# Optimization experiments

Hardware: AMD Instinct MI355X
Metric: run time of the kernel (lower is better)

The kernel has to match this reference:

```python
import jax, jax.numpy as jnp
import numpy as np

TEMPERATURE = 8.0  # sqrt(head_dim=64)


def setup_inputs() -> dict:
    key = jax.random.key(0)
    kq, kk, kv, km = jax.random.split(key, 4)
    B, S, D = 16, 2048, 64
    q = jax.random.normal(kq, (B, S, D), dtype=jnp.float32)
    k = jax.random.normal(kk, (B, S, D), dtype=jnp.float32)
    v = jax.random.normal(kv, (B, S, D), dtype=jnp.float32)
    mask = jax.random.randint(km, (B, S, S), 0, 2).astype(jnp.bool_)
    return {"q": q, "k": k, "v": v, "mask": mask}


def reference(q, k, v, mask):
    # latent = q @ k^T / temperature  -> [B, Sq, Sk]
    latent = jnp.einsum('bqd,bkd->bqk', q, k) / TEMPERATURE
    # NOTE: the original fills masked positions with 1e-9 (NOT -inf); keep faithful.
    latent = jnp.where(mask, jnp.float32(1e-9), latent)
    attn = jax.nn.softmax(latent, axis=-1)
    return jnp.einsum('bqk,bkd->bqd', attn, v)
```

## Files before the change

### kernel.cpp

```cpp
#include <hip/hip_runtime.h>
#include <hip/hip_bf16.h>

#define BB 16
#define SS 2048
#define DD 64

typedef __attribute__((ext_vector_type(8)))  unsigned short ushort8;
typedef __attribute__((ext_vector_type(8)))  __bf16 bf16x8;
typedef __attribute__((ext_vector_type(16))) float f32x16;

static __device__ __forceinline__ unsigned short f2bf(float x) {
    return __builtin_bit_cast(unsigned short, __float2bfloat16(x));
}
static __device__ __forceinline__ unsigned pk2(float a, float b) {
    return (unsigned)f2bf(a) | ((unsigned)f2bf(b) << 16);
}
union F4 { float4 v; float a[4]; };

__global__ __launch_bounds__(256, 4)
void sdpa_mfma_kernel(const float* __restrict__ Q, const float* __restrict__ K,
                      const float* __restrict__ V, const unsigned int* __restrict__ M,
                      float* __restrict__ O) {
    __shared__ __align__(16) char smem[37120];
    char* Ks = smem;
    char* Vs = smem + 16384;
    char* Ms = smem + 32768;
    char* Qs = smem + 32768;
    float* red  = (float*)smem;
    float* denx = (float*)(smem + 32768);

    const int t    = threadIdx.x;
    const int lane = t & 63;
    const int l31  = lane & 31;
    const int half = lane >> 5;
    const int kh   = t >> 6;
    const int b    = blockIdx.y;
    const int q0   = blockIdx.x * 32;

    const float* Kg = K + (size_t)b * SS * DD;
    const float* Vg = V + (size_t)b * SS * DD;
    const unsigned int* Mg = M + (size_t)b * SS * SS + (size_t)q0 * SS;

    {
        const int sr = t >> 3, sc = t & 7;
        const float* src = Q + ((size_t)b * SS + q0 + sr) * DD + sc * 8;
        F4 f0, f1; f0.v = *(const float4*)src; f1.v = *(const float4*)(src + 4);
        ushort8 u;
        #pragma unroll
        for (int e = 0; e < 4; e++) {
            u[e]     = f2bf(f0.a[e] * 0.125f);
            u[e + 4] = f2bf(f1.a[e] * 0.125f);
        }
        *(ushort8*)(Qs + sr * 128 + ((sc ^ (sr & 7)) * 16)) = u;
    }
    __syncthreads();

    const int qrow = l31;
    bf16x8 bq[4];
    #pragma unroll
    for (int dc = 0; dc < 4; dc++)
        bq[dc] = __builtin_bit_cast(bf16x8, *(const ushort8*)(
            Qs + qrow * 128 + (((2 * dc + half) ^ (qrow & 7)) * 16)));
    __syncthreads();

    f32x16 On0, On1;
    #pragma unroll
    for (int i = 0; i < 16; i++) { On0[i] = 0.f; On1[i] = 0.f; }
    float den_acc = 0.f;

    const int krow = 32 * kh + l31;
    const int d0v  = (t & 15) * 4;
    const int kkb  = (t >> 4) * 4;

    for (int kt = 0; kt < SS / 128; ++kt) {
        #pragma unroll
        for (int j = 0; j < 4; j++) {
            const int idx = 2 * t + 512 * j;
            const int row = idx >> 4;
            const int g   = (idx & 15) >> 1;
            const float* src = Kg + (size_t)(kt * 128) * DD + (size_t)idx * 4;
            F4 fa, fb; fa.v = *(const float4*)src; fb.v = *(const float4*)(src + 4);
            ushort8 u;
            #pragma unroll
            for (int e = 0; e < 4; e++) { u[e] = f2bf(fa.a[e]); u[e + 4] = f2bf(fb.a[e]); }
            *(ushort8*)(Ks + row * 128 + ((g ^ (row & 7)) * 16)) = u;
        }
        #pragma unroll
        for (int it2 = 0; it2 < 2; it2++) {
            const int kk = kkb + 64 * it2;
            const float* src = Vg + (size_t)(kt * 128 + kk) * DD + d0v;
            F4 r0, r1, r2, r3;
            r0.v = *(const float4*)(src);
            r1.v = *(const float4*)(src + DD);
            r2.v = *(const float4*)(src + 2 * DD);
            r3.v = *(const float4*)(src + 3 * DD);
            #pragma unroll
            for (int e = 0; e < 4; e++) {
                const int d = d0v + e;
                const uint2 wv = make_uint2(pk2(r0.a[e], r1.a[e]), pk2(r2.a[e], r3.a[e]));
                *(uint2*)(Vs + d * 256 + (((kk >> 3) ^ (d & 15)) * 16) + (kk & 7) * 2) = wv;
            }
        }
        {
            const int sr = t >> 3, sc = t & 7;
            const unsigned int* Mw = Mg + (size_t)sr * SS + kt * 128 + sc * 16;
            unsigned wd[4];
            #pragma unroll
            for (int g = 0; g < 4; g++) {
                const uint4 u = *(const uint4*)(Mw + 4 * g);
                wd[g] = (u.x ? 1u : 0u) | (u.y ? 0x100u : 0u) |
                        (u.z ? 0x10000u : 0u) | (u.w ? 0x1000000u : 0u);
            }
            *(uint2*)(Ms + sr * 136 + sc * 16)     = make_uint2(wd[0], wd[1]);
            *(uint2*)(Ms + sr * 136 + sc * 16 + 8) = make_uint2(wd[2], wd[3]);
        }
        __syncthreads();

        f32x16 S;
        #pragma unroll
        for (int i = 0; i < 16; i++) S[i] = 0.f;
        #pragma unroll
        for (int dc = 0; dc < 4; dc++) {
            bf16x8 ak = __builtin_bit_cast(bf16x8, *(const ushort8*)(
                Ks + krow * 128 + (((2 * dc + half) ^ (krow & 7)) * 16)));
            S = __builtin_amdgcn_mfma_f32_32x32x16_bf16(ak, bq[dc], S, 0, 0, 0);
        }

        float p[16];
        #pragma unroll
        for (int g = 0; g < 4; g++) {
            const unsigned mw = *(const unsigned*)(Ms + qrow * 136 + 32 * kh + 8 * g + 4 * half);
            #pragma unroll
            for (int e = 0; e < 4; e++) {
                const float ev = __expf(S[4 * g + e]);
                const float pv = ((mw >> (8 * e)) & 0xffu) ? 1.0f : ev;
                p[4 * g + e] = pv;
                den_acc += pv;
            }
        }

        #pragma unroll
        for (int s2 = 0; s2 < 2; s2++) {
            const unsigned o0 = pk2(p[8 * s2 + 0], p[8 * s2 + 1]);
            const unsigned o1 = pk2(p[8 * s2 + 2], p[8 * s2 + 3]);
            const unsigned o2 = pk2(p[8 * s2 + 4], p[8 * s2 + 5]);
            const unsigned o3 = pk2(p[8 * s2 + 6], p[8 * s2 + 7]);
            const unsigned s0 = half ? o0 : o2;
            const unsigned s1 = half ? o1 : o3;
            const unsigned r0 = (unsigned)__shfl_xor((int)s0, 32, 64);
            const unsigned r1 = (unsigned)__shfl_xor((int)s1, 32, 64);
            uint4 bu;
            bu.x = half ? r0 : o0;
            bu.y = half ? r1 : o1;
            bu.z = half ? o2 : r0;
            bu.w = half ? o3 : r1;
            const bf16x8 bp = __builtin_bit_cast(bf16x8, bu);
            #pragma unroll
            for (int dc = 0; dc < 2; dc++) {
                const int vrow = 32 * dc + l31;
                bf16x8 av = __builtin_bit_cast(bf16x8, *(const ushort8*)(
                    Vs + vrow * 256 + (((4 * kh + 2 * s2 + half) ^ (vrow & 15)) * 16)));
                if (dc == 0) On0 = __builtin_amdgcn_mfma_f32_32x32x16_bf16(av, bp, On0, 0, 0, 0);
                else         On1 = __builtin_amdgcn_mfma_f32_32x32x16_bf16(av, bp, On1, 0, 0, 0);
            }
        }
        __syncthreads();
    }

    const float den_tot = den_acc + __shfl_xor(den_acc, 32, 64);

    __syncthreads();
    if (kh != 0) {
        #pragma unroll
        for (int dc = 0; dc < 2; dc++)
            #pragma unroll
            for (int g = 0; g < 4; g++) {
                const f32x16& Oc = dc ? On1 : On0;
                float4 st;
                st.x = Oc[4 * g + 0]; st.y = Oc[4 * g + 1];
                st.z = Oc[4 * g + 2]; st.w = Oc[4 * g + 3];
                *(float4*)((char*)red + (kh - 1) * 8192 + (dc * 4 + g) * 1024 + lane * 16) = st;
            }
        if (lane < 32) denx[kh * 32 + l31] = den_tot;
    }
    __syncthreads();
    if (kh == 0) {
        const float inv = 1.0f / (den_tot + denx[32 + l31] + denx[64 + l31] + denx[96 + l31]);
        float* Og = O + ((size_t)b * SS + q0 + qrow) * DD;
        #pragma unroll
        for (int dc = 0; dc < 2; dc++)
            #pragma unroll
            for (int g = 0; g < 4; g++) {
                const f32x16& Oc = dc ? On1 : On0;
                float4 st;
                st.x = Oc[4 * g + 0]; st.y = Oc[4 * g + 1];
                st.z = Oc[4 * g + 2]; st.w = Oc[4 * g + 3];
                #pragma unroll
                for (int w2 = 0; w2 < 3; w2++) {
                    const float4 pr = *(const float4*)((char*)red + w2 * 8192 +
                                                       (dc * 4 + g) * 1024 + lane * 16);
                    st.x += pr.x; st.y += pr.y; st.z += pr.z; st.w += pr.w;
                }
                st.x *= inv; st.y *= inv; st.z *= inv; st.w *= inv;
                *(float4*)(Og + 32 * dc + 8 * g + 4 * half) = st;
            }
    }
}

extern "C" void kernel_launch(void* const* d_in, const int* in_sizes, int n_in,
                              void* d_out, int out_size, void* d_ws, size_t ws_size,
                              hipStream_t stream) {
    const float* q = (const float*)d_in[0];
    const float* k = (const float*)d_in[1];
    const float* v = (const float*)d_in[2];
    const unsigned int* m = (const unsigned int*)d_in[3];
    float* out = (float*)d_out;

    dim3 grid(SS / 32, BB);
    sdpa_mfma_kernel<<<grid, 256, 0, stream>>>(q, k, v, m, out);
}
```

Before: 402.8 us.

## Prepack K/V to swizzled bf16 tiles and stream them via global_load_lds

A new prepack kernel converts K and V once into bf16 tiles already laid out with the LDS swizzle and stores them in the workspace. The attention kernel then copies each tile straight into LDS with global_load_lds instead of reconverting fp32 K/V in every one of the 64 query blocks per batch. The mask reads become nontemporal loads so the large mask stream does not pollute the cache. This costs an extra launch and workspace traffic, and the direct-to-LDS path has to match the expected layout exactly.

```diff
diff --git a/kernel.cpp b/kernel.cpp
--- a/kernel.cpp
+++ b/kernel.cpp
@@ -4,10 +4,13 @@
 #define BB 16
 #define SS 2048
 #define DD 64
+#define NT_TILES (SS / 128)
+#define TILE_BYTES 16384
 
 typedef __attribute__((ext_vector_type(8)))  unsigned short ushort8;
 typedef __attribute__((ext_vector_type(8)))  __bf16 bf16x8;
 typedef __attribute__((ext_vector_type(16))) float f32x16;
+typedef __attribute__((ext_vector_type(4)))  unsigned int uint4v;
 
 static __device__ __forceinline__ unsigned short f2bf(float x) {
     return __builtin_bit_cast(unsigned short, __float2bfloat16(x));
@@ -17,9 +20,67 @@
 }
 union F4 { float4 v; float a[4]; };
 
+#define GLDS16(src, dst) __builtin_amdgcn_global_load_lds(                 \
+    (const __attribute__((address_space(1))) unsigned int*)(src),          \
+    (__attribute__((address_space(3))) unsigned int*)(dst), 16, 0, 0)
+
+__global__ __launch_bounds__(256)
+void prepack_kernel(const float* __restrict__ K, const float* __restrict__ V,
+                    char* __restrict__ wsK, char* __restrict__ wsV) {
+    __shared__ __align__(16) char smem[32768];
+    char* Ks = smem;
+    char* Vs = smem + 16384;
+    const int t  = threadIdx.x;
+    const int kt = blockIdx.x;
+    const int b  = blockIdx.y;
+    const float* Kg = K + (size_t)b * SS * DD;
+    const float* Vg = V + (size_t)b * SS * DD;
+
+    #pragma unroll
+    for (int j = 0; j < 4; j++) {
+        const int idx = 2 * t + 512 * j;
+        const int row = idx >> 4;
+        const int g   = (idx & 15) >> 1;
+        const float* src = Kg + (size_t)(kt * 128) * DD + (size_t)idx * 4;
+        F4 fa, fb; fa.v = *(const float4*)src; fb.v = *(const float4*)(src + 4);
+        ushort8 u;
+        #pragma unroll
+        for (int e = 0; e < 4; e++) { u[e] = f2bf(fa.a[e]); u[e + 4] = f2bf(fb.a[e]); }
+        *(ushort8*)(Ks + row * 128 + ((g ^ (row & 7)) * 16)) = u;
+    }
+    {
+        const int d0v = (t & 15) * 4;
+        const int kkb = (t >> 4) * 4;
+        #pragma unroll
+        for (int it2 = 0; it2 < 2; it2++) {
+            const int kk = kkb + 64 * it2;
+            const float* src = Vg + (size_t)(kt * 128 + kk) * DD + d0v;
+            F4 r0, r1, r2, r3;
+            r0.v = *(const float4*)(src);
+            r1.v = *(const float4*)(src + DD);
+            r2.v = *(const float4*)(src + 2 * DD);
+            r3.v = *(const float4*)(src + 3 * DD);
+            #pragma unroll
+            for (int e = 0; e < 4; e++) {
+                const int d = d0v + e;
+                const uint2 wv = make_uint2(pk2(r0.a[e], r1.a[e]), pk2(r2.a[e], r3.a[e]));
+                *(uint2*)(Vs + d * 256 + (((kk >> 3) ^ (d & 15)) * 16) + (kk & 7) * 2) = wv;
+            }
+        }
+    }
+    __syncthreads();
+    char* dK = wsK + (size_t)(b * NT_TILES + kt) * TILE_BYTES;
+    char* dV = wsV + (size_t)(b * NT_TILES + kt) * TILE_BYTES;
+    #pragma unroll
+    for (int j = 0; j < 4; j++) {
+        *(float4*)(dK + t * 16 + j * 4096) = *(const float4*)(Ks + t * 16 + j * 4096);
+        *(float4*)(dV + t * 16 + j * 4096) = *(const float4*)(Vs + t * 16 + j * 4096);
+    }
+}
+
 __global__ __launch_bounds__(256, 4)
-void sdpa_mfma_kernel(const float* __restrict__ Q, const float* __restrict__ K,
-                      const float* __restrict__ V, const unsigned int* __restrict__ M,
+void sdpa_mfma_kernel(const float* __restrict__ Q, const char* __restrict__ wsK,
+                      const char* __restrict__ wsV, const unsigned int* __restrict__ M,
                       float* __restrict__ O) {
     __shared__ __align__(16) char smem[37120];
     char* Ks = smem;
@@ -37,8 +98,6 @@
     const int b    = blockIdx.y;
     const int q0   = blockIdx.x * 32;
 
-    const float* Kg = K + (size_t)b * SS * DD;
-    const float* Vg = V + (size_t)b * SS * DD;
     const unsigned int* Mg = M + (size_t)b * SS * SS + (size_t)q0 * SS;
 
     {
@@ -69,37 +128,14 @@
     float den_acc = 0.f;
 
     const int krow = 32 * kh + l31;
-    const int d0v  = (t & 15) * 4;
-    const int kkb  = (t >> 4) * 4;
-
-    for (int kt = 0; kt < SS / 128; ++kt) {
+
+    for (int kt = 0; kt < NT_TILES; ++kt) {
+        const char* tK = wsK + (size_t)(b * NT_TILES + kt) * TILE_BYTES;
+        const char* tV = wsV + (size_t)(b * NT_TILES + kt) * TILE_BYTES;
         #pragma unroll
         for (int j = 0; j < 4; j++) {
-            const int idx = 2 * t + 512 * j;
-            const int row = idx >> 4;
-            const int g   = (idx & 15) >> 1;
-            const float* src = Kg + (size_t)(kt * 128) * DD + (size_t)idx * 4;
-            F4 fa, fb; fa.v = *(const float4*)src; fb.v = *(const float4*)(src + 4);
-            ushort8 u;
-            #pragma unroll
-            for (int e = 0; e < 4; e++) { u[e] = f2bf(fa.a[e]); u[e + 4] = f2bf(fb.a[e]); }
-            *(ushort8*)(Ks + row * 128 + ((g ^ (row & 7)) * 16)) = u;
-        }
-        #pragma unroll
-        for (int it2 = 0; it2 < 2; it2++) {
-            const int kk = kkb + 64 * it2;
-            const float* src = Vg + (size_t)(kt * 128 + kk) * DD + d0v;
-            F4 r0, r1, r2, r3;
-            r0.v = *(const float4*)(src);
-            r1.v = *(const float4*)(src + DD);
-            r2.v = *(const float4*)(src + 2 * DD);
-            r3.v = *(const float4*)(src + 3 * DD);
-            #pragma unroll
-            for (int e = 0; e < 4; e++) {
-                const int d = d0v + e;
-                const uint2 wv = make_uint2(pk2(r0.a[e], r1.a[e]), pk2(r2.a[e], r3.a[e]));
-                *(uint2*)(Vs + d * 256 + (((kk >> 3) ^ (d & 15)) * 16) + (kk & 7) * 2) = wv;
-            }
+            GLDS16(tK + t * 16 + j * 4096, Ks + kh * 1024 + j * 4096);
+            GLDS16(tV + t * 16 + j * 4096, Vs + kh * 1024 + j * 4096);
         }
         {
             const int sr = t >> 3, sc = t & 7;
@@ -107,9 +143,9 @@
             unsigned wd[4];
             #pragma unroll
             for (int g = 0; g < 4; g++) {
-                const uint4 u = *(const uint4*)(Mw + 4 * g);
-                wd[g] = (u.x ? 1u : 0u) | (u.y ? 0x100u : 0u) |
-                        (u.z ? 0x10000u : 0u) | (u.w ? 0x1000000u : 0u);
+                const uint4v u = __builtin_nontemporal_load((const uint4v*)(Mw + 4 * g));
+                wd[g] = (u[0] ? 1u : 0u) | (u[1] ? 0x100u : 0u) |
+                        (u[2] ? 0x10000u : 0u) | (u[3] ? 0x1000000u : 0u);
             }
             *(uint2*)(Ms + sr * 136 + sc * 16)     = make_uint2(wd[0], wd[1]);
             *(uint2*)(Ms + sr * 136 + sc * 16 + 8) = make_uint2(wd[2], wd[3]);
@@ -216,6 +252,12 @@
     const unsigned int* m = (const unsigned int*)d_in[3];
     float* out = (float*)d_out;
 
+    char* wsK = (char*)d_ws;
+    char* wsV = (char*)d_ws + (size_t)BB * NT_TILES * TILE_BYTES;
+
+    dim3 pgrid(NT_TILES, BB);
+    prepack_kernel<<<pgrid, 256, 0, stream>>>(k, v, wsK, wsV);
+
     dim3 grid(SS / 32, BB);
-    sdpa_mfma_kernel<<<grid, 256, 0, stream>>>(q, k, v, m, out);
-}
+    sdpa_mfma_kernel<<<grid, 256, 0, stream>>>(q, wsK, wsV, m, out);
+}
```

New measurement: 412.6 us. +2.4%, slower.
